# Optimization experiments

Measured on AMD Instinct MI355X. Metric: run time of the kernel, lower is better.

The kernel has to match this reference:

```python
import jax, jax.numpy as jnp
import numpy as np

FRAMES = 8
NUM_HEADS = 12


def _build_indices_mask(N_origin):
    """Static (numpy) construction of gathered token indices and the
    multiplicative token mask (1.0 on allowed pairs, 0.8 elsewhere),
    matching token_mask + (1-token_mask)*0.8 in the torch code."""
    N = FRAMES * N_origin
    cls_idx = np.arange(0, N, N_origin)
    per_frame = [np.arange(i * N_origin + 1 + i, (i + 1) * N_origin, FRAMES)
                 for i in range(FRAMES)]
    idx = np.concatenate([cls_idx] + per_frame)
    M = idx.shape[0]
    mask = np.full((N, M), 0.8, dtype=np.float32)
    cls_len = cls_idx.shape[0]
    mask[:, :cls_len] = 1.0
    st = cls_len
    for i in range(FRAMES):
        ln = per_frame[i].shape[0]
        mask[i * N_origin:(i + 1) * N_origin, st:st + ln] = 1.0
        st += ln
    return jnp.asarray(idx), jnp.asarray(mask)


def setup_inputs() -> dict:
    key = jax.random.key(0)
    k1, k2, k3, k4 = jax.random.split(key, 4)
    C = 768
    x = jax.random.normal(k1, (64, 197, C), dtype=jnp.float32)
    qkv_w = jax.random.normal(k2, (3 * C, C), dtype=jnp.float32) * 0.02
    proj_w = jax.random.normal(k3, (C, C), dtype=jnp.float32) * 0.02
    proj_b = jax.random.normal(k4, (C,), dtype=jnp.float32) * 0.02
    return {"x": x, "qkv_w": qkv_w, "proj_w": proj_w, "proj_b": proj_b}


def reference(x, qkv_w, proj_w, proj_b):
    B0, N_origin, C = x.shape
    H = NUM_HEADS
    hd = C // H
    B = B0 // FRAMES
    N = FRAMES * N_origin
    scale = hd ** -0.5

    xg = x.reshape(B, N, C)                              # group 8 frames per video
    qkv = (xg @ qkv_w.T).reshape(B, N, 3, H, hd).transpose(2, 0, 3, 1, 4)
    q, k, v = qkv[0], qkv[1], qkv[2]                     # each [B, H, N, hd]

    idx, mask = _build_indices_mask(N_origin)            # idx [M], mask [N, M]
    k = k[:, :, idx, :]                                  # [B, H, M, hd]
    v = v[:, :, idx, :]

    attn = jnp.einsum('bhnd,bhmd->bhnm', q, k) * scale   # [B, H, N, M]
    attn = jax.nn.softmax(attn * mask, axis=-1)          # multiplicative mask, then softmax

    out = jnp.einsum('bhnm,bhmd->bhnd', attn, v)         # [B, H, N, hd]
    out = out.transpose(0, 2, 1, 3).reshape(B, N, C)
    out = out @ proj_w.T + proj_b
    return out.reshape(B0, N_origin, C)
```

## Files before the change

### kernel.cpp

```cpp
#include <hip/hip_runtime.h>
#include <stdint.h>

#define NORI   197
#define FRAMES 8
#define NTOK   1576
#define BATCH  8
#define NHEAD  12
#define CDIM   768
#define MG     204
#define TOKENS 12608

typedef _Float16 half8 __attribute__((ext_vector_type(8)));
typedef float floatx4 __attribute__((ext_vector_type(4)));

typedef const __attribute__((address_space(1))) void GPTR;
typedef __attribute__((address_space(3))) void LPTR;

__device__ __forceinline__ int gather_idx(int m) {
    if (m < 8) return m * NORI;
    int u = m - 8;
    int f, t;
    if (u < 100) { f = u / 25; t = u - f * 25; }
    else         { f = 4 + (u - 100) / 24; t = (u - 100) - (f - 4) * 24; }
    return f * NORI + 1 + f + 8 * t;
}
__device__ __forceinline__ int col_frame(int m) {
    int u = m - 8;
    return (u < 100) ? (u / 25) : (4 + (u - 100) / 24);
}

__global__ __launch_bounds__(256) void cast_all(
    const float* __restrict__ x, const float* __restrict__ qkvw,
    const float* __restrict__ projw, _Float16* __restrict__ out)
{
    const int n1 = TOKENS * CDIM / 8, n2 = 3 * CDIM * CDIM / 8, n3 = CDIM * CDIM / 8;
    int i = blockIdx.x * 256 + threadIdx.x;
    if (i >= n1 + n2 + n3) return;
    const float* src; int off;
    if (i < n1)           { src = x;     off = i; }
    else if (i < n1 + n2) { src = qkvw;  off = i - n1; }
    else                  { src = projw; off = i - n1 - n2; }
    float4 a = ((const float4*)src)[2 * off];
    float4 b = ((const float4*)src)[2 * off + 1];
    half8 o = { (_Float16)a.x, (_Float16)a.y, (_Float16)a.z, (_Float16)a.w,
                (_Float16)b.x, (_Float16)b.y, (_Float16)b.z, (_Float16)b.w };
    ((half8*)out)[i] = o;
}

template <int OUT_F32>
__device__ __forceinline__ void gemm_body(
    const _Float16* __restrict__ A, const _Float16* __restrict__ W,
    const float* __restrict__ bias, void* __restrict__ Y,
    int M, int Woff, int ldY, int gather, int r0, int c0,
    _Float16* As, _Float16* Bs)
{
    const int tid = threadIdx.x;
    const int w = tid >> 6, l = tid & 63;
    const int wm = (w >> 1) * 64, wn = (w & 1) * 64;

    const int pos = l & 7, rsub = l >> 3;
    const int cg = pos ^ rsub;

    const _Float16* sa[4];
    const _Float16* sb[4];
    _Float16* lA[4];
    _Float16* lB[4];
#pragma unroll
    for (int i = 0; i < 4; i++) {
        int rt = w * 32 + i * 8 + rsub;
        int ra = min(r0 + rt, M - 1);
        if (gather) { int b = ra / MG; int m = ra - b * MG; ra = b * NTOK + gather_idx(m); }
        sa[i] = A + (size_t)ra * CDIM + cg * 8;
        sb[i] = W + (size_t)(Woff + c0 + rt) * CDIM + cg * 8;
        lA[i] = &As[(w * 32 + i * 8) * 64];
        lB[i] = &Bs[(w * 32 + i * 8) * 64];
    }

    floatx4 acc[4][4] = {};
    const int mrow = l & 15, lq = l >> 4;

    for (int kb = 0; kb < CDIM; kb += 64) {
        __syncthreads();
#pragma unroll
        for (int i = 0; i < 4; i++) {
            __builtin_amdgcn_global_load_lds((GPTR*)(sa[i] + kb), (LPTR*)lA[i], 16, 0, 0);
            __builtin_amdgcn_global_load_lds((GPTR*)(sb[i] + kb), (LPTR*)lB[i], 16, 0, 0);
        }
        __syncthreads();

#pragma unroll
        for (int ksi = 0; ksi < 2; ksi++) {
            half8 af[4], bf[4];
#pragma unroll
            for (int t = 0; t < 4; t++) {
                af[t] = *(const half8*)&As[(wm + t * 16 + mrow) * 64 + (((ksi * 4 + lq)) ^ (mrow & 7)) * 8];
                bf[t] = *(const half8*)&Bs[(wn + t * 16 + mrow) * 64 + (((ksi * 4 + lq)) ^ (mrow & 7)) * 8];
            }
#pragma unroll
            for (int mt = 0; mt < 4; mt++)
#pragma unroll
                for (int nt = 0; nt < 4; nt++)
                    acc[mt][nt] = __builtin_amdgcn_mfma_f32_16x16x32_f16(af[mt], bf[nt], acc[mt][nt], 0, 0, 0);
        }
    }

#pragma unroll
    for (int nt = 0; nt < 4; nt++) {
        int col = c0 + wn + nt * 16 + (l & 15);
        float bv = bias ? bias[col] : 0.f;
#pragma unroll
        for (int mt = 0; mt < 4; mt++) {
#pragma unroll
            for (int r = 0; r < 4; r++) {
                int row = r0 + wm + mt * 16 + (l >> 4) * 4 + r;
                if (row < M) {
                    if (OUT_F32) ((float*)Y)[(size_t)row * ldY + col] = acc[mt][nt][r] + bv;
                    else ((_Float16*)Y)[(size_t)row * ldY + col] = (_Float16)acc[mt][nt][r];
                }
            }
        }
    }
}

__global__ __launch_bounds__(256) void gemm_qkv(
    const _Float16* __restrict__ xh, const _Float16* __restrict__ qkvwh,
    _Float16* __restrict__ Qh, _Float16* __restrict__ KVh)
{
    __shared__ __align__(16) _Float16 As[128 * 64];
    __shared__ __align__(16) _Float16 Bs[128 * 64];
    int bx = blockIdx.x;
    if (bx < 594) {
        gemm_body<0>(xh, qkvwh, nullptr, Qh, TOKENS, 0, CDIM, 0,
                     (bx / 6) * 128, (bx % 6) * 128, As, Bs);
    } else {
        int b2 = bx - 594;
        gemm_body<0>(xh, qkvwh, nullptr, KVh, BATCH * MG, CDIM, 1536, 1,
                     (b2 / 12) * 128, (b2 % 12) * 128, As, Bs);
    }
}

__global__ __launch_bounds__(256) void gemm_proj(
    const _Float16* __restrict__ AOh, const _Float16* __restrict__ projwh,
    const float* __restrict__ bias, float* __restrict__ out)
{
    __shared__ __align__(16) _Float16 As[128 * 64];
    __shared__ __align__(16) _Float16 Bs[128 * 64];
    int bx = blockIdx.x;
    gemm_body<1>(AOh, projwh, bias, out, TOKENS, 0, CDIM, 0,
                 (bx / 6) * 128, (bx % 6) * 128, As, Bs);
}

__global__ __launch_bounds__(256, 2) void attn_mfma(
    const _Float16* __restrict__ Qh, const _Float16* __restrict__ KVh,
    _Float16* __restrict__ AOh)
{
    __shared__ __align__(16) _Float16 Ks[204 * 64];
    __shared__ __align__(16) _Float16 Vt[64 * 208];
    __shared__ __align__(16) _Float16 Ps[64 * 216];

    const int tid = threadIdx.x;
    const int bh = blockIdx.x;
    const int b = bh / NHEAD, h = bh - b * NHEAD;
    const int qc0 = blockIdx.y * 320;

    for (int e = tid; e < MG * 8; e += 256) {
        int row = e >> 3, c8 = e & 7;
        half8 v = *(const half8*)&KVh[(size_t)(b * MG + row) * 1536 + h * 64 + c8 * 8];
        *(half8*)&Ks[row * 64 + ((c8 ^ (row & 7)) * 8)] = v;
    }
    {
        const int d0 = (tid >> 5) * 8, lmp = tid & 31;
#pragma unroll
        for (int mo = 0; mo < 7; mo++) {
            int mp = mo * 32 + lmp;
            if (mp >= 208) continue;
            half8 v = {};
            if (mp < MG) v = *(const half8*)&KVh[(size_t)(b * MG + mp) * 1536 + 768 + h * 64 + d0];
#pragma unroll
            for (int j = 0; j < 8; j++) Vt[(d0 + j) * 208 + mp] = v[j];
        }
    }
    __syncthreads();

    const int w = tid >> 6, l = tid & 63;
    const int lm = l & 15, lq = l >> 4;

    int cf[13];
#pragma unroll
    for (int t = 0; t < 13; t++) {
        int col = t * 16 + lm;
        cf[t] = (col < 8) ? -1 : (col >= MG ? -2 : col_frame(col));
    }

    _Float16* Pw = &Ps[(w * 16) * 216];

    for (int t5 = 0; t5 < 5; t5++) {
        const int rb = qc0 + t5 * 64 + w * 16;
        if (rb >= NTOK) break;

        floatx4 acc[13] = {};
        const int qrowA = min(rb + lm, NTOK - 1);
        const _Float16* qbase = Qh + (size_t)(b * NTOK + qrowA) * CDIM + h * 64;
#pragma unroll
        for (int ks = 0; ks < 64; ks += 32) {
            half8 aq = *(const half8*)(qbase + ks + lq * 8);
#pragma unroll
            for (int t = 0; t < 13; t++) {
                half8 bk = *(const half8*)&Ks[(t * 16 + lm) * 64 + (((ks >> 3) + lq) ^ (lm & 7)) * 8];
                acc[t] = __builtin_amdgcn_mfma_f32_16x16x32_f16(aq, bk, acc[t], 0, 0, 0);
            }
        }

#pragma unroll
        for (int r = 0; r < 4; r++) {
            int qrow = min(rb + lq * 4 + r, NTOK - 1);
            int rf = qrow / NORI;
            float sv[13];
            float mx = -1e30f;
#pragma unroll
            for (int t = 0; t < 13; t++) {
                float s = acc[t][r] * 0.125f;
                s *= (cf[t] == -1 || cf[t] == rf) ? 1.f : 0.8f;
                if (cf[t] == -2) s = -1e30f;
                sv[t] = s;
                mx = fmaxf(mx, s);
            }
#pragma unroll
            for (int off = 1; off < 16; off <<= 1) mx = fmaxf(mx, __shfl_xor(mx, off, 64));
            float sum = 0.f;
#pragma unroll
            for (int t = 0; t < 13; t++) { sv[t] = __expf(sv[t] - mx); sum += sv[t]; }
#pragma unroll
            for (int off = 1; off < 16; off <<= 1) sum += __shfl_xor(sum, off, 64);
            float inv = 1.f / sum;
#pragma unroll
            for (int t = 0; t < 13; t++) acc[t][r] = sv[t] * inv;
        }

#pragma unroll
        for (int t = 0; t < 13; t++)
#pragma unroll
            for (int r = 0; r < 4; r++)
                Pw[(lq * 4 + r) * 216 + t * 16 + lm] = (_Float16)acc[t][r];

        floatx4 oacc[4] = {};
        const _Float16* prow = &Pw[lm * 216];
#pragma unroll
        for (int ks = 0; ks < 192; ks += 32) {
            half8 ap = *(const half8*)(prow + ks + lq * 8);
#pragma unroll
            for (int t = 0; t < 4; t++) {
                half8 bv = *(const half8*)&Vt[(t * 16 + lm) * 208 + ks + lq * 8];
                oacc[t] = __builtin_amdgcn_mfma_f32_16x16x32_f16(ap, bv, oacc[t], 0, 0, 0);
            }
        }
        {
            typedef _Float16 half4v __attribute__((ext_vector_type(4)));
            half4v ap4 = *(const half4v*)(prow + 192 + lq * 4);
#pragma unroll
            for (int t = 0; t < 4; t++) {
                half4v bv4 = *(const half4v*)&Vt[(t * 16 + lm) * 208 + 192 + lq * 4];
                oacc[t] = __builtin_amdgcn_mfma_f32_16x16x16f16(ap4, bv4, oacc[t], 0, 0, 0);
            }
        }

#pragma unroll
        for (int t = 0; t < 4; t++)
#pragma unroll
            for (int r = 0; r < 4; r++) {
                int qrow = rb + lq * 4 + r;
                if (qrow < NTOK)
                    AOh[(size_t)(b * NTOK + qrow) * CDIM + h * 64 + t * 16 + lm] = (_Float16)oacc[t][r];
            }
    }
}

extern "C" void kernel_launch(void* const* d_in, const int* in_sizes, int n_in,
                              void* d_out, int out_size, void* d_ws, size_t ws_size,
                              hipStream_t stream) {
    const float* x      = (const float*)d_in[0];
    const float* qkv_w  = (const float*)d_in[1];
    const float* proj_w = (const float*)d_in[2];
    const float* proj_b = (const float*)d_in[3];
    float* out = (float*)d_out;

    _Float16* xh     = (_Float16*)d_ws;
    _Float16* qkvwh  = xh + (size_t)TOKENS * CDIM;
    _Float16* projwh = qkvwh + (size_t)3 * CDIM * CDIM;
    _Float16* Qh     = projwh + (size_t)CDIM * CDIM;
    _Float16* KVh    = Qh + (size_t)TOKENS * CDIM;
    _Float16* AOh    = KVh + (size_t)(BATCH * MG) * 1536;

    dim3 blk(256);
    const int ncast = (TOKENS * CDIM + 3 * CDIM * CDIM + CDIM * CDIM) / 8;
    cast_all<<<dim3((ncast + 255) / 256), blk, 0, stream>>>(x, qkv_w, proj_w, xh);

    gemm_qkv<<<dim3(594 + 156), blk, 0, stream>>>(xh, qkvwh, Qh, KVh);

    attn_mfma<<<dim3(BATCH * NHEAD, 5), blk, 0, stream>>>(Qh, KVh, AOh);

    gemm_proj<<<dim3(594), blk, 0, stream>>>(AOh, projwh, proj_b, out);
}
```

Before: 201.9 us.

## Double-buffer GEMM LDS tiles and remap blocks across XCDs for L2 reuse

The GEMM main loop now uses two LDS buffers. The next K-slice is loaded with global_load_lds while the current one feeds MFMA, synchronised by explicit waitcnt and barriers, so load latency overlaps compute. Blocks are also remapped so consecutive row blocks land on the same XCD, aiming for better L2 reuse of the A rows. This doubles LDS per block to 64KB, which can lower occupancy, and adds idle padded blocks that exit early.

```diff
diff --git a/kernel.cpp b/kernel.cpp
--- a/kernel.cpp
+++ b/kernel.cpp
@@ -52,7 +52,7 @@
     const _Float16* __restrict__ A, const _Float16* __restrict__ W,
     const float* __restrict__ bias, void* __restrict__ Y,
     int M, int Woff, int ldY, int gather, int r0, int c0,
-    _Float16* As, _Float16* Bs)
+    _Float16* As0, _Float16* Bs0, _Float16* As1, _Float16* Bs1)
 {
     const int tid = threadIdx.x;
     const int w = tid >> 6, l = tid & 63;
@@ -63,8 +63,7 @@
 
     const _Float16* sa[4];
     const _Float16* sb[4];
-    _Float16* lA[4];
-    _Float16* lB[4];
+    int soff[4];
 #pragma unroll
     for (int i = 0; i < 4; i++) {
         int rt = w * 32 + i * 8 + rsub;
@@ -72,29 +71,45 @@
         if (gather) { int b = ra / MG; int m = ra - b * MG; ra = b * NTOK + gather_idx(m); }
         sa[i] = A + (size_t)ra * CDIM + cg * 8;
         sb[i] = W + (size_t)(Woff + c0 + rt) * CDIM + cg * 8;
-        lA[i] = &As[(w * 32 + i * 8) * 64];
-        lB[i] = &Bs[(w * 32 + i * 8) * 64];
+        soff[i] = (w * 32 + i * 8) * 64;
+    }
+
+#pragma unroll
+    for (int i = 0; i < 4; i++) {
+        __builtin_amdgcn_global_load_lds((GPTR*)sa[i], (LPTR*)(As0 + soff[i]), 16, 0, 0);
+        __builtin_amdgcn_global_load_lds((GPTR*)sb[i], (LPTR*)(Bs0 + soff[i]), 16, 0, 0);
     }
 
     floatx4 acc[4][4] = {};
     const int mrow = l & 15, lq = l >> 4;
 
-    for (int kb = 0; kb < CDIM; kb += 64) {
-        __syncthreads();
-#pragma unroll
-        for (int i = 0; i < 4; i++) {
-            __builtin_amdgcn_global_load_lds((GPTR*)(sa[i] + kb), (LPTR*)lA[i], 16, 0, 0);
-            __builtin_amdgcn_global_load_lds((GPTR*)(sb[i] + kb), (LPTR*)lB[i], 16, 0, 0);
-        }
-        __syncthreads();
+#pragma unroll
+    for (int it = 0; it < 12; it++) {
+        const _Float16* Ac = (it & 1) ? As1 : As0;
+        const _Float16* Bc = (it & 1) ? Bs1 : Bs0;
+        _Float16* An = (it & 1) ? As0 : As1;
+        _Float16* Bn = (it & 1) ? Bs0 : Bs1;
+
+        if (it < 11) {
+            int kb = (it + 1) * 64;
+#pragma unroll
+            for (int i = 0; i < 4; i++) {
+                __builtin_amdgcn_global_load_lds((GPTR*)(sa[i] + kb), (LPTR*)(An + soff[i]), 16, 0, 0);
+                __builtin_amdgcn_global_load_lds((GPTR*)(sb[i] + kb), (LPTR*)(Bn + soff[i]), 16, 0, 0);
+            }
+            __builtin_amdgcn_s_waitcnt(0x0078);
+        } else {
+            __builtin_amdgcn_s_waitcnt(0x0070);
+        }
+        __builtin_amdgcn_s_barrier();
 
 #pragma unroll
         for (int ksi = 0; ksi < 2; ksi++) {
             half8 af[4], bf[4];
 #pragma unroll
             for (int t = 0; t < 4; t++) {
-                af[t] = *(const half8*)&As[(wm + t * 16 + mrow) * 64 + (((ksi * 4 + lq)) ^ (mrow & 7)) * 8];
-                bf[t] = *(const half8*)&Bs[(wn + t * 16 + mrow) * 64 + (((ksi * 4 + lq)) ^ (mrow & 7)) * 8];
+                af[t] = *(const half8*)&Ac[(wm + t * 16 + mrow) * 64 + ((ksi * 4 + lq) ^ (mrow & 7)) * 8];
+                bf[t] = *(const half8*)&Bc[(wn + t * 16 + mrow) * 64 + ((ksi * 4 + lq) ^ (mrow & 7)) * 8];
             }
 #pragma unroll
             for (int mt = 0; mt < 4; mt++)
@@ -102,6 +117,7 @@
                 for (int nt = 0; nt < 4; nt++)
                     acc[mt][nt] = __builtin_amdgcn_mfma_f32_16x16x32_f16(af[mt], bf[nt], acc[mt][nt], 0, 0, 0);
         }
+        __builtin_amdgcn_s_barrier();
     }
 
 #pragma unroll
@@ -122,20 +138,31 @@
     }
 }
 
+__device__ __forceinline__ bool xcd_map(int bx, int nrb, int& rb, int& cb) {
+    int xcd = bx & 7, j = bx >> 3;
+    rb = (j % 13) * 8 + xcd;
+    cb = j / 13;
+    return rb < nrb;
+}
+
 __global__ __launch_bounds__(256) void gemm_qkv(
     const _Float16* __restrict__ xh, const _Float16* __restrict__ qkvwh,
     _Float16* __restrict__ Qh, _Float16* __restrict__ KVh)
 {
-    __shared__ __align__(16) _Float16 As[128 * 64];
-    __shared__ __align__(16) _Float16 Bs[128 * 64];
+    __shared__ __align__(16) _Float16 As0[128 * 64];
+    __shared__ __align__(16) _Float16 Bs0[128 * 64];
+    __shared__ __align__(16) _Float16 As1[128 * 64];
+    __shared__ __align__(16) _Float16 Bs1[128 * 64];
     int bx = blockIdx.x;
-    if (bx < 594) {
+    if (bx < 624) {
+        int rb, cb;
+        if (!xcd_map(bx, 99, rb, cb)) return;
         gemm_body<0>(xh, qkvwh, nullptr, Qh, TOKENS, 0, CDIM, 0,
-                     (bx / 6) * 128, (bx % 6) * 128, As, Bs);
+                     rb * 128, cb * 128, As0, Bs0, As1, Bs1);
     } else {
-        int b2 = bx - 594;
+        int b2 = bx - 624;
         gemm_body<0>(xh, qkvwh, nullptr, KVh, BATCH * MG, CDIM, 1536, 1,
-                     (b2 / 12) * 128, (b2 % 12) * 128, As, Bs);
+                     (b2 / 12) * 128, (b2 % 12) * 128, As0, Bs0, As1, Bs1);
     }
 }
 
@@ -143,11 +170,14 @@
     const _Float16* __restrict__ AOh, const _Float16* __restrict__ projwh,
     const float* __restrict__ bias, float* __restrict__ out)
 {
-    __shared__ __align__(16) _Float16 As[128 * 64];
-    __shared__ __align__(16) _Float16 Bs[128 * 64];
-    int bx = blockIdx.x;
+    __shared__ __align__(16) _Float16 As0[128 * 64];
+    __shared__ __align__(16) _Float16 Bs0[128 * 64];
+    __shared__ __align__(16) _Float16 As1[128 * 64];
+    __shared__ __align__(16) _Float16 Bs1[128 * 64];
+    int rb, cb;
+    if (!xcd_map(blockIdx.x, 99, rb, cb)) return;
     gemm_body<1>(AOh, projwh, bias, out, TOKENS, 0, CDIM, 0,
-                 (bx / 6) * 128, (bx % 6) * 128, As, Bs);
+                 rb * 128, cb * 128, As0, Bs0, As1, Bs1);
 }
 
 __global__ __launch_bounds__(256, 2) void attn_mfma(
@@ -295,9 +325,9 @@
     const int ncast = (TOKENS * CDIM + 3 * CDIM * CDIM + CDIM * CDIM) / 8;
     cast_all<<<dim3((ncast + 255) / 256), blk, 0, stream>>>(x, qkv_w, proj_w, xh);
 
-    gemm_qkv<<<dim3(594 + 156), blk, 0, stream>>>(xh, qkvwh, Qh, KVh);
+    gemm_qkv<<<dim3(624 + 156), blk, 0, stream>>>(xh, qkvwh, Qh, KVh);
 
     attn_mfma<<<dim3(BATCH * NHEAD, 5), blk, 0, stream>>>(Qh, KVh, AOh);
 
-    gemm_proj<<<dim3(594), blk, 0, stream>>>(AOh, projwh, proj_b, out);
-}
+    gemm_proj<<<dim3(624), blk, 0, stream>>>(AOh, projwh, proj_b, out);
+}
```

New measurement: 191.4 us. 1.06x faster.
